# Performance work log

Hardware: AMD Instinct MI355X
Metric: run time of the kernel (lower is better)

## Reference

```python
import math
import jax, jax.numpy as jnp
import numpy as np

B, C, T = 4, 512, 1024
H = 8
KC = C // H
WIN = 4


def _get_relative_embeddings(emb, length):
    win = (emb.shape[1] - 1) // 2
    pad_length = max(length - (win + 1), 0)
    slice_start = max(win + 1 - length, 0)
    slice_end = slice_start + 2 * length - 1
    if pad_length > 0:
        emb = jnp.pad(emb, ((0, 0), (pad_length, pad_length), (0, 0)))
    return emb[:, slice_start:slice_end]


def _relative_to_absolute(x):
    # x: [b, h, L, 2L-1] -> [b, h, L, L] via skew trick
    b, h, L, _ = x.shape
    x = jnp.pad(x, ((0, 0), (0, 0), (0, 0), (0, 1)))          # [b,h,L,2L]
    x_flat = x.reshape(b, h, L * 2 * L)
    x_flat = jnp.pad(x_flat, ((0, 0), (0, 0), (0, L - 1)))    # [b,h,(L+1)(2L-1)]
    x_final = x_flat.reshape(b, h, L + 1, 2 * L - 1)
    return x_final[:, :, :L, L - 1:]


def _absolute_to_relative(x):
    # x: [b, h, L, L] -> [b, h, L, 2L-1]
    b, h, L, _ = x.shape
    x = jnp.pad(x, ((0, 0), (0, 0), (0, 0), (0, L - 1)))      # [b,h,L,2L-1]
    x_flat = x.reshape(b, h, L * (2 * L - 1))
    x_flat = jnp.pad(x_flat, ((0, 0), (0, 0), (L, 0)))        # [b,h,2L^2]
    x_final = x_flat.reshape(b, h, L, 2 * L)
    return x_final[:, :, :, 1:]


def setup_inputs() -> dict:
    key = jax.random.key(0)
    ks = jax.random.split(key, 12)
    xavier = math.sqrt(6.0 / (C + C))  # xavier_uniform for [C, C, 1] conv weight
    rel_std = KC ** (-0.5)
    return {
        "x": jax.random.normal(ks[0], (B, C, T), dtype=jnp.float32),
        "wq": jax.random.uniform(ks[1], (C, C), jnp.float32, -xavier, xavier),
        "bq": jnp.zeros((C,), jnp.float32),
        "wk": jax.random.uniform(ks[2], (C, C), jnp.float32, -xavier, xavier),
        "bk": jnp.zeros((C,), jnp.float32),
        "wv": jax.random.uniform(ks[3], (C, C), jnp.float32, -xavier, xavier),
        "bv": jnp.zeros((C,), jnp.float32),
        "wo": jax.random.normal(ks[4], (C, C), jnp.float32) * (1.0 / math.sqrt(C)),
        "bo": jnp.zeros((C,), jnp.float32),
        "emb_rel_k": jax.random.normal(ks[5], (1, 2 * WIN + 1, KC), jnp.float32) * rel_std,
        "emb_rel_v": jax.random.normal(ks[6], (1, 2 * WIN + 1, KC), jnp.float32) * rel_std,
    }


def reference(x, wq, bq, wk, bk, wv, bv, wo, bo, emb_rel_k, emb_rel_v):
    b, c, t = x.shape
    # 1x1 conv == channel matmul
    q = jnp.einsum("oi,bit->bot", wq, x) + bq[:, None]
    k = jnp.einsum("oi,bit->bot", wk, x) + bk[:, None]
    v = jnp.einsum("oi,bit->bot", wv, x) + bv[:, None]
    # [b, H, t, kc]
    q = q.reshape(b, H, KC, t).transpose(0, 1, 3, 2)
    k = k.reshape(b, H, KC, t).transpose(0, 1, 3, 2)
    v = v.reshape(b, H, KC, t).transpose(0, 1, 3, 2)
    inv_sqrt = 1.0 / math.sqrt(KC)
    scores = jnp.einsum("bhtc,bhsc->bhts", q, k) * inv_sqrt
    rel_k = _get_relative_embeddings(emb_rel_k, t)[0]            # [2t-1, kc]
    rel_logits = jnp.einsum("bhtc,rc->bhtr", q, rel_k)           # [b,h,t,2t-1]
    scores = scores + _relative_to_absolute(rel_logits) * inv_sqrt
    p_attn = jax.nn.softmax(scores, axis=-1)
    output = jnp.einsum("bhts,bhsc->bhtc", p_attn, v)
    rel_weights = _absolute_to_relative(p_attn)                  # [b,h,t,2t-1]
    rel_v = _get_relative_embeddings(emb_rel_v, t)[0]            # [2t-1, kc]
    output = output + jnp.einsum("bhtr,rc->bhtc", rel_weights, rel_v)
    output = output.transpose(0, 1, 3, 2).reshape(b, c, t)
    return jnp.einsum("oi,bit->bot", wo, output) + bo[:, None]
```

## Files before the change

kernel.cpp:

```cpp
#include <hip/hip_runtime.h>
#include <hip/hip_bf16.h>

#define Bdim 4
#define Cdim 512
#define Tdim 1024
#define Hn   8
#define KCd  64

typedef __attribute__((ext_vector_type(8))) short bf16x8;
typedef __attribute__((ext_vector_type(4))) float f32x4;

__device__ __forceinline__ unsigned short f32_bf16_rne(float f) {
    unsigned u = __float_as_uint(f);
    u += 0x7FFFu + ((u >> 16) & 1u);
    return (unsigned short)(u >> 16);
}
__device__ __forceinline__ float bf16_f32(unsigned short h) {
    return __uint_as_float(((unsigned)h) << 16);
}

__device__ __forceinline__ int off_row(int row, int c) {
    return (((row >> 4) * 2 + (c >> 5)) << 9)
         + (((((c >> 3) & 3) << 4) + (row & 15)) << 3) + (c & 7);
}
__device__ __forceinline__ int off_col(int c, int j) {
    return (((c >> 4) * 2 + (j >> 5)) << 9)
         + (((((j >> 3) & 3) << 4) + (c & 15)) << 3) + (j & 7);
}

__device__ __forceinline__ int sw(int row, int col) {
    return (row << 6) + ((((col >> 3) ^ (row & 7)) << 3) | (col & 7));
}
__device__ __forceinline__ bf16x8 fragld(const unsigned short* a, int row, int kstep, int quad) {
    return *(const bf16x8*)&a[(row << 6) + ((((kstep << 2) | quad) ^ (row & 7)) << 3)];
}

#define BM 128
#define BN 64
#define BK 32
#define LDK 40

__global__ __launch_bounds__(256) void gemm3_mfma(
    int mode,
    const float* __restrict__ w0, const float* __restrict__ w1, const float* __restrict__ w2,
    const float* __restrict__ b0, const float* __restrict__ b1, const float* __restrict__ b2,
    const float* __restrict__ x,
    unsigned short* __restrict__ qhi, unsigned short* __restrict__ qlo,
    unsigned short* __restrict__ khi, unsigned short* __restrict__ klo,
    unsigned short* __restrict__ vhi, unsigned short* __restrict__ vlo,
    float* __restrict__ ofp)
{
    __shared__ unsigned short Whi[BM][LDK], Wlo[BM][LDK];
    __shared__ unsigned short Xhi[BN][LDK], Xlo[BN][LDK];

    const int tid = threadIdx.x;

    int bx, by, b;
    {
        const int n = blockIdx.x;
        const int xcd = n & 7, slot = n >> 3;
        if (mode == 0) {
            const int stripe = (xcd << 3) | (slot / 12);
            by = slot % 12;
            bx = stripe & 15;
            b  = stripe >> 4;
        } else {
            const int stripe = (xcd << 3) | (slot >> 2);
            by = slot & 3;
            bx = stripe & 15;
            b  = stripe >> 4;
        }
    }

    const int m_tile = by * BM;
    const int sel = m_tile >> 9;
    const float* W  = sel == 0 ? w0 : (sel == 1 ? w1 : w2);
    const float* Bv = sel == 0 ? b0 : (sel == 1 ? b1 : b2);
    const int m0 = m_tile & 511;
    const int n0 = bx * BN;

    const float* Xb = x + (size_t)b * Cdim * Tdim;

    const int lane = tid & 63, wid = tid >> 6;
    const int wm = (wid & 1) * 64, wn = (wid >> 1) * 32;
    const int l15 = lane & 15, quad = lane >> 4;

    const int wk4 = (tid & 7) * 4;
    const int wmr = tid >> 3;
    const int xn  = tid & 63;
    const int xo  = tid >> 6;

    f32x4 acc[4][2];
    #pragma unroll
    for (int i = 0; i < 4; ++i)
        #pragma unroll
        for (int j = 0; j < 2; ++j) acc[i][j] = (f32x4){0.f, 0.f, 0.f, 0.f};

    for (int k0 = 0; k0 < Cdim; k0 += BK) {
        __syncthreads();

        #pragma unroll
        for (int p = 0; p < 4; ++p) {
            const int m = wmr + p * 32;
            float4 wv = *(const float4*)(W + (size_t)(m0 + m) * Cdim + k0 + wk4);
            ushort4 hi, lo;
            hi.x = f32_bf16_rne(wv.x); lo.x = f32_bf16_rne(wv.x - bf16_f32(hi.x));
            hi.y = f32_bf16_rne(wv.y); lo.y = f32_bf16_rne(wv.y - bf16_f32(hi.y));
            hi.z = f32_bf16_rne(wv.z); lo.z = f32_bf16_rne(wv.z - bf16_f32(hi.z));
            hi.w = f32_bf16_rne(wv.w); lo.w = f32_bf16_rne(wv.w - bf16_f32(hi.w));
            *(ushort4*)&Whi[m][wk4] = hi;
            *(ushort4*)&Wlo[m][wk4] = lo;
        }

        {
            float xv[8];
            #pragma unroll
            for (int kk = 0; kk < 8; ++kk)
                xv[kk] = Xb[(size_t)(k0 + xo * 8 + kk) * Tdim + n0 + xn];
            ushort4 hi0, hi1, lo0, lo1;
            unsigned short h;
            h = f32_bf16_rne(xv[0]); hi0.x = h; lo0.x = f32_bf16_rne(xv[0] - bf16_f32(h));
            h = f32_bf16_rne(xv[1]); hi0.y = h; lo0.y = f32_bf16_rne(xv[1] - bf16_f32(h));
            h = f32_bf16_rne(xv[2]); hi0.z = h; lo0.z = f32_bf16_rne(xv[2] - bf16_f32(h));
            h = f32_bf16_rne(xv[3]); hi0.w = h; lo0.w = f32_bf16_rne(xv[3] - bf16_f32(h));
            h = f32_bf16_rne(xv[4]); hi1.x = h; lo1.x = f32_bf16_rne(xv[4] - bf16_f32(h));
            h = f32_bf16_rne(xv[5]); hi1.y = h; lo1.y = f32_bf16_rne(xv[5] - bf16_f32(h));
            h = f32_bf16_rne(xv[6]); hi1.z = h; lo1.z = f32_bf16_rne(xv[6] - bf16_f32(h));
            h = f32_bf16_rne(xv[7]); hi1.w = h; lo1.w = f32_bf16_rne(xv[7] - bf16_f32(h));
            *(ushort4*)&Xhi[xn][xo * 8]     = hi0;
            *(ushort4*)&Xhi[xn][xo * 8 + 4] = hi1;
            *(ushort4*)&Xlo[xn][xo * 8]     = lo0;
            *(ushort4*)&Xlo[xn][xo * 8 + 4] = lo1;
        }
        __syncthreads();

        bf16x8 ahi[4], alo[4], bhi[2], blo[2];
        #pragma unroll
        for (int mt = 0; mt < 4; ++mt) {
            ahi[mt] = *(const bf16x8*)&Whi[wm + mt * 16 + l15][quad * 8];
            alo[mt] = *(const bf16x8*)&Wlo[wm + mt * 16 + l15][quad * 8];
        }
        #pragma unroll
        for (int nt = 0; nt < 2; ++nt) {
            bhi[nt] = *(const bf16x8*)&Xhi[wn + nt * 16 + l15][quad * 8];
            blo[nt] = *(const bf16x8*)&Xlo[wn + nt * 16 + l15][quad * 8];
        }
        #pragma unroll
        for (int mt = 0; mt < 4; ++mt)
            #pragma unroll
            for (int nt = 0; nt < 2; ++nt) {
                f32x4 c = acc[mt][nt];
                c = __builtin_amdgcn_mfma_f32_16x16x32_bf16(ahi[mt], bhi[nt], c, 0, 0, 0);
                c = __builtin_amdgcn_mfma_f32_16x16x32_bf16(ahi[mt], blo[nt], c, 0, 0, 0);
                c = __builtin_amdgcn_mfma_f32_16x16x32_bf16(alo[mt], bhi[nt], c, 0, 0, 0);
                acc[mt][nt] = c;
            }
    }

    if (mode == 1) {
        float* Ob = ofp + (size_t)b * Cdim * Tdim;
        #pragma unroll
        for (int mt = 0; mt < 4; ++mt) {
            const int mb = m0 + wm + mt * 16 + quad * 4;
            float bb[4];
            #pragma unroll
            for (int r = 0; r < 4; ++r) bb[r] = Bv[mb + r];
            #pragma unroll
            for (int nt = 0; nt < 2; ++nt) {
                const int t = n0 + wn + nt * 16 + l15;
                #pragma unroll
                for (int r = 0; r < 4; ++r)
                    Ob[(size_t)(mb + r) * Tdim + t] = acc[mt][nt][r] + bb[r];
            }
        }
    } else if (sel < 2) {
        unsigned short* phi = sel == 0 ? qhi : khi;
        unsigned short* plo = sel == 0 ? qlo : klo;
        #pragma unroll
        for (int mt = 0; mt < 4; ++mt) {
            const int mv = m0 + wm + mt * 16 + quad * 4;
            const int head = mv >> 6, c0 = mv & 63;
            float bb[4];
            #pragma unroll
            for (int r = 0; r < 4; ++r) bb[r] = Bv[mv + r];
            #pragma unroll
            for (int nt = 0; nt < 2; ++nt) {
                const int t = n0 + wn + nt * 16 + l15;
                const int tile = t >> 6, r_ = t & 63;
                const size_t off = (((size_t)(b * Hn + head) * 16 + tile) << 12)
                                 + (size_t)off_row(r_, c0);
                ushort4 h4, l4;
                float v0 = acc[mt][nt][0] + bb[0];
                float v1 = acc[mt][nt][1] + bb[1];
                float v2 = acc[mt][nt][2] + bb[2];
                float v3 = acc[mt][nt][3] + bb[3];
                h4.x = f32_bf16_rne(v0); l4.x = f32_bf16_rne(v0 - bf16_f32(h4.x));
                h4.y = f32_bf16_rne(v1); l4.y = f32_bf16_rne(v1 - bf16_f32(h4.y));
                h4.z = f32_bf16_rne(v2); l4.z = f32_bf16_rne(v2 - bf16_f32(h4.z));
                h4.w = f32_bf16_rne(v3); l4.w = f32_bf16_rne(v3 - bf16_f32(h4.w));
                *(ushort4*)(phi + off) = h4;
                *(ushort4*)(plo + off) = l4;
            }
        }
    } else {
        #pragma unroll
        for (int mt = 0; mt < 4; ++mt) {
            const int mv = m0 + wm + mt * 16 + quad * 4;
            const int head = mv >> 6;
            float bb[4];
            #pragma unroll
            for (int r = 0; r < 4; ++r) bb[r] = Bv[mv + r];
            #pragma unroll
            for (int nt = 0; nt < 2; ++nt) {
                const int t = n0 + wn + nt * 16 + l15;
                const int tile = t >> 6, jl = t & 63;
                const size_t tb = ((size_t)(b * Hn + head) * 16 + tile) << 12;
                #pragma unroll
                for (int r = 0; r < 4; ++r) {
                    const int cr = (mv & 63) + r;
                    const float v = acc[mt][nt][r] + bb[r];
                    const unsigned short h = f32_bf16_rne(v);
                    const size_t off = tb + off_col(cr, jl);
                    vhi[off] = h;
                    vlo[off] = f32_bf16_rne(v - bf16_f32(h));
                }
            }
        }
    }
}

__global__ __launch_bounds__(256) void attn_mfma(
    const unsigned short* __restrict__ qhi, const unsigned short* __restrict__ qlo,
    const unsigned short* __restrict__ khi, const unsigned short* __restrict__ klo,
    const unsigned short* __restrict__ vhi, const unsigned short* __restrict__ vlo,
    const float* __restrict__ ek,
    const float* __restrict__ ev,
    float* __restrict__ ctx)
{
    __shared__ alignas(16) unsigned short psh[4096], psl[4096];
    __shared__ float rk[576];
    __shared__ float evs[576];

    const int tid = threadIdx.x;

    int it, h, b;
    {
        const int n = blockIdx.x;
        const int xcd = n & 7, slot = n >> 3;
        const int pair = (xcd << 2) | (slot >> 4);
        it = slot & 15;
        b = pair >> 3;
        h = pair & 7;
    }
    const int i0 = it * 64;
    const int lane = tid & 63, w = tid >> 6;
    const int l15 = lane & 15, quad = lane >> 4;
    const int m_blk = w * 16 + l15;
    const int lo8 = lane << 3;

    const size_t bh16 = (size_t)(b * Hn + h) * 16;
    float* ctxb = ctx + ((size_t)b * Cdim + h * KCd) * Tdim;

    bf16x8 qfh[2], qfl[2];
    {
        const unsigned short* qth = qhi + ((bh16 + it) << 12);
        const unsigned short* qtl = qlo + ((bh16 + it) << 12);
        #pragma unroll
        for (int ks = 0; ks < 2; ++ks) {
            qfh[ks] = *(const bf16x8*)(qth + (((w << 1) | ks) << 9) + lo8);
            qfl[ks] = *(const bf16x8*)(qtl + (((w << 1) | ks) << 9) + lo8);
        }
    }

    bf16x8 ekh[2], ekl[2];
    #pragma unroll
    for (int ks = 0; ks < 2; ++ks) {
        #pragma unroll
        for (int j = 0; j < 8; ++j) { ekh[ks][j] = 0; ekl[ks][j] = 0; }
        if (l15 < 9) {
            #pragma unroll
            for (int j = 0; j < 8; ++j) {
                const float v = ek[l15 * 64 + ks * 32 + quad * 8 + j];
                const unsigned short hh = f32_bf16_rne(v);
                ekh[ks][j] = (short)hh;
                ekl[ks][j] = (short)f32_bf16_rne(v - bf16_f32(hh));
            }
        }
    }

    {
        f32x4 rkD = (f32x4){0.f, 0.f, 0.f, 0.f};
        #pragma unroll
        for (int ks = 0; ks < 2; ++ks) {
            rkD = __builtin_amdgcn_mfma_f32_16x16x32_bf16(qfh[ks], ekh[ks], rkD, 0, 0, 0);
            rkD = __builtin_amdgcn_mfma_f32_16x16x32_bf16(qfh[ks], ekl[ks], rkD, 0, 0, 0);
            rkD = __builtin_amdgcn_mfma_f32_16x16x32_bf16(qfl[ks], ekh[ks], rkD, 0, 0, 0);
        }
        if (l15 < 9) {
            #pragma unroll
            for (int r = 0; r < 4; ++r)
                rk[(w * 16 + quad * 4 + r) * 9 + l15] = rkD[r];
        }
    }
    for (int idx = tid; idx < 576; idx += 256) evs[idx] = ev[idx];
    __syncthreads();

    float m_run = -1e30f, l_run = 0.f;
    f32x4 Oc[4];
    #pragma unroll
    for (int ct = 0; ct < 4; ++ct) Oc[ct] = (f32x4){0.f, 0.f, 0.f, 0.f};

    const unsigned short* kh0 = khi + (bh16 << 12);
    const unsigned short* kl0 = klo + (bh16 << 12);
    const unsigned short* vh0 = vhi + (bh16 << 12);
    const unsigned short* vl0 = vlo + (bh16 << 12);

    for (int t = 0; t < 16; ++t) {
        const int j0 = t << 6;
        const size_t tb = (size_t)t << 12;
        const unsigned short* kht = kh0 + tb;
        const unsigned short* klt = kl0 + tb;
        const unsigned short* vht = vh0 + tb;
        const unsigned short* vlt = vl0 + tb;

        bf16x8 vbh[2][4], vbl[2][4];
        #pragma unroll
        for (int ks = 0; ks < 2; ++ks)
            #pragma unroll
            for (int ct = 0; ct < 4; ++ct) {
                vbh[ks][ct] = *(const bf16x8*)(vht + (((ct << 1) | ks) << 9) + lo8);
                vbl[ks][ct] = *(const bf16x8*)(vlt + (((ct << 1) | ks) << 9) + lo8);
            }

        f32x4 Sc[4];
        #pragma unroll
        for (int jt = 0; jt < 4; ++jt) Sc[jt] = (f32x4){0.f, 0.f, 0.f, 0.f};
        #pragma unroll
        for (int ks = 0; ks < 2; ++ks) {
            bf16x8 ah[4], al[4];
            #pragma unroll
            for (int jt = 0; jt < 4; ++jt) {
                ah[jt] = *(const bf16x8*)(kht + (((jt << 1) | ks) << 9) + lo8);
                al[jt] = *(const bf16x8*)(klt + (((jt << 1) | ks) << 9) + lo8);
            }
            #pragma unroll
            for (int jt = 0; jt < 4; ++jt) {
                Sc[jt] = __builtin_amdgcn_mfma_f32_16x16x32_bf16(ah[jt], qfh[ks], Sc[jt], 0, 0, 0);
                Sc[jt] = __builtin_amdgcn_mfma_f32_16x16x32_bf16(ah[jt], qfl[ks], Sc[jt], 0, 0, 0);
                Sc[jt] = __builtin_amdgcn_mfma_f32_16x16x32_bf16(al[jt], qfh[ks], Sc[jt], 0, 0, 0);
            }
        }

        const int dt = j0 - i0;
        const bool diag = (dt >= -67 && dt <= 67);
        if (diag) {
            #pragma unroll
            for (int jt = 0; jt < 4; ++jt) {
                const int db = dt + jt * 16 + quad * 4 - m_blk;
                #pragma unroll
                for (int r = 0; r < 4; ++r) {
                    const int d = db + r;
                    if ((unsigned)(d + 4) <= 8u) Sc[jt][r] += rk[m_blk * 9 + d + 4];
                }
            }
        }

        float mt = -1e30f;
        #pragma unroll
        for (int jt = 0; jt < 4; ++jt)
            #pragma unroll
            for (int r = 0; r < 4; ++r) {
                Sc[jt][r] *= 0.125f;
                mt = fmaxf(mt, Sc[jt][r]);
            }
        mt = fmaxf(mt, __shfl_xor(mt, 16));
        mt = fmaxf(mt, __shfl_xor(mt, 32));
        const float mn = fmaxf(m_run, mt);
        const float alpha = __expf(m_run - mn);
        float rs = 0.f;
        #pragma unroll
        for (int jt = 0; jt < 4; ++jt)
            #pragma unroll
            for (int r = 0; r < 4; ++r) {
                const float e = __expf(Sc[jt][r] - mn);
                Sc[jt][r] = e;
                rs += e;
            }
        rs += __shfl_xor(rs, 16);
        rs += __shfl_xor(rs, 32);
        l_run = l_run * alpha + rs;
        m_run = mn;

        #pragma unroll
        for (int jt = 0; jt < 4; ++jt) {
            ushort4 ph, pl;
            ph.x = f32_bf16_rne(Sc[jt][0]); pl.x = f32_bf16_rne(Sc[jt][0] - bf16_f32(ph.x));
            ph.y = f32_bf16_rne(Sc[jt][1]); pl.y = f32_bf16_rne(Sc[jt][1] - bf16_f32(ph.y));
            ph.z = f32_bf16_rne(Sc[jt][2]); pl.z = f32_bf16_rne(Sc[jt][2] - bf16_f32(ph.z));
            ph.w = f32_bf16_rne(Sc[jt][3]); pl.w = f32_bf16_rne(Sc[jt][3] - bf16_f32(ph.w));
            const int o = sw(m_blk, jt * 16 + quad * 4);
            *(ushort4*)&psh[o] = ph;
            *(ushort4*)&psl[o] = pl;
        }

        const float al0 = __shfl(alpha, quad * 4 + 0);
        const float al1 = __shfl(alpha, quad * 4 + 1);
        const float al2 = __shfl(alpha, quad * 4 + 2);
        const float al3 = __shfl(alpha, quad * 4 + 3);
        #pragma unroll
        for (int ct = 0; ct < 4; ++ct) {
            Oc[ct][0] *= al0; Oc[ct][1] *= al1; Oc[ct][2] *= al2; Oc[ct][3] *= al3;
        }
        #pragma unroll
        for (int ks = 0; ks < 2; ++ks) {
            bf16x8 pah = fragld(psh, m_blk, ks, quad);
            bf16x8 pal = fragld(psl, m_blk, ks, quad);
            #pragma unroll
            for (int ct = 0; ct < 4; ++ct) {
                Oc[ct] = __builtin_amdgcn_mfma_f32_16x16x32_bf16(pah, vbh[ks][ct], Oc[ct], 0, 0, 0);
                Oc[ct] = __builtin_amdgcn_mfma_f32_16x16x32_bf16(pah, vbl[ks][ct], Oc[ct], 0, 0, 0);
                Oc[ct] = __builtin_amdgcn_mfma_f32_16x16x32_bf16(pal, vbh[ks][ct], Oc[ct], 0, 0, 0);
            }
        }

        if (diag) {
            #pragma unroll
            for (int r = 0; r < 4; ++r) {
                const int mrow = w * 16 + quad * 4 + r;
                const int ig = i0 + mrow;
                #pragma unroll
                for (int e = 0; e < 9; ++e) {
                    const int jl = ig + e - 4 - j0;
                    if ((unsigned)jl < 64u) {
                        const int o = sw(mrow, jl);
                        const float p = bf16_f32(psh[o]) + bf16_f32(psl[o]);
                        #pragma unroll
                        for (int ct = 0; ct < 4; ++ct)
                            Oc[ct][r] += p * evs[e * 64 + ct * 16 + l15];
                    }
                }
            }
        }
    }

    const float rlv = 1.f / l_run;
    const float rl0 = __shfl(rlv, quad * 4 + 0);
    const float rl1 = __shfl(rlv, quad * 4 + 1);
    const float rl2 = __shfl(rlv, quad * 4 + 2);
    const float rl3 = __shfl(rlv, quad * 4 + 3);
    #pragma unroll
    for (int ct = 0; ct < 4; ++ct) {
        float4 o4;
        o4.x = Oc[ct][0] * rl0;
        o4.y = Oc[ct][1] * rl1;
        o4.z = Oc[ct][2] * rl2;
        o4.w = Oc[ct][3] * rl3;
        *(float4*)(ctxb + (size_t)(ct * 16 + l15) * Tdim + i0 + w * 16 + quad * 4) = o4;
    }
}

extern "C" void kernel_launch(void* const* d_in, const int* in_sizes, int n_in,
                              void* d_out, int out_size, void* d_ws, size_t ws_size,
                              hipStream_t stream) {
    const float* x  = (const float*)d_in[0];
    const float* wq = (const float*)d_in[1];
    const float* bq = (const float*)d_in[2];
    const float* wk = (const float*)d_in[3];
    const float* bk = (const float*)d_in[4];
    const float* wv = (const float*)d_in[5];
    const float* bv = (const float*)d_in[6];
    const float* wo = (const float*)d_in[7];
    const float* bo = (const float*)d_in[8];
    const float* ek = (const float*)d_in[9];
    const float* ev = (const float*)d_in[10];
    float* out = (float*)d_out;

    const size_t plane = (size_t)Bdim * Cdim * Tdim;
    unsigned short* qhi = (unsigned short*)d_ws;
    unsigned short* qlo = qhi + plane;
    unsigned short* khi = qlo + plane;
    unsigned short* klo = khi + plane;
    unsigned short* vhi = klo + plane;
    unsigned short* vlo = vhi + plane;
    float* cbuf = (float*)(vlo + plane);

    gemm3_mfma<<<dim3(768), 256, 0, stream>>>(
        0, wq, wk, wv, bq, bk, bv, x, qhi, qlo, khi, klo, vhi, vlo, nullptr);

    attn_mfma<<<dim3(512), 256, 0, stream>>>(
        qhi, qlo, khi, klo, vhi, vlo, ek, ev, cbuf);

    gemm3_mfma<<<dim3(256), 256, 0, stream>>>(
        1, wo, wo, wo, bo, bo, bo, cbuf,
        nullptr, nullptr, nullptr, nullptr, nullptr, nullptr, out);
}
```

Before: 182.8 us.

## Pre-split operands into MFMA fragment layout and drop LDS staging in GEMMs

Adds a prep kernel that converts all four weight matrices and x into hi/lo bf16 pairs, stored directly in MFMA fragment order. The projection GEMMs then load fragments straight from global memory with register double-buffering, and each wave computes a 64x64 tile with no shared memory or barriers. The attention kernel now writes its context as pre-split bf16 fragments, so the output projection also skips conversion. The cost is an extra launch plus more global traffic. Occupancy is lower (384 and 128 blocks), and the weights are re-split on every call.

```diff
diff --git a/kernel.cpp b/kernel.cpp
--- a/kernel.cpp
+++ b/kernel.cpp
@@ -18,14 +18,13 @@
 __device__ __forceinline__ float bf16_f32(unsigned short h) {
     return __uint_as_float(((unsigned)h) << 16);
 }
-
-__device__ __forceinline__ int off_row(int row, int c) {
-    return (((row >> 4) * 2 + (c >> 5)) << 9)
-         + (((((c >> 3) & 3) << 4) + (row & 15)) << 3) + (c & 7);
-}
-__device__ __forceinline__ int off_col(int c, int j) {
-    return (((c >> 4) * 2 + (j >> 5)) << 9)
-         + (((((j >> 3) & 3) << 4) + (c & 15)) << 3) + (j & 7);
+__device__ __forceinline__ void split8(const float* f, bf16x8& h8, bf16x8& l8) {
+    #pragma unroll
+    for (int e = 0; e < 8; ++e) {
+        const unsigned short hh = f32_bf16_rne(f[e]);
+        h8[e] = (short)hh;
+        l8[e] = (short)f32_bf16_rne(f[e] - bf16_f32(hh));
+    }
 }
 
 __device__ __forceinline__ int sw(int row, int col) {
@@ -35,124 +34,132 @@
     return *(const bf16x8*)&a[(row << 6) + ((((kstep << 2) | quad) ^ (row & 7)) << 3)];
 }
 
-#define BM 128
-#define BN 64
-#define BK 32
-#define LDK 40
-
-__global__ __launch_bounds__(256) void gemm3_mfma(
+
+__global__ __launch_bounds__(256) void prep_kernel(
+    const float* __restrict__ wq, const float* __restrict__ wk,
+    const float* __restrict__ wv, const float* __restrict__ wo,
+    const float* __restrict__ x,
+    unsigned short* __restrict__ WAhi, unsigned short* __restrict__ WAlo,
+    unsigned short* __restrict__ XBhi, unsigned short* __restrict__ XBlo)
+{
+    const int w = threadIdx.x >> 6, lane = threadIdx.x & 63;
+    const int l15 = lane & 15, quad = lane >> 4;
+    const int task = blockIdx.x * 4 + w;
+
+    if (task < 2048) {
+        const int mtile = task >> 4, kt = task & 15;
+        const int sel = mtile >> 5;
+        const float* W = sel == 0 ? wq : (sel == 1 ? wk : (sel == 2 ? wv : wo));
+        const int row = (mtile & 31) * 16 + l15;
+        const float* p = W + (size_t)row * Cdim + kt * 32 + quad * 8;
+        float f[8];
+        *(float4*)&f[0] = *(const float4*)p;
+        *(float4*)&f[4] = *(const float4*)(p + 4);
+        bf16x8 h8, l8;
+        split8(f, h8, l8);
+        const size_t base = (size_t)task * 512 + lane * 8;
+        *(bf16x8*)(WAhi + base) = h8;
+        *(bf16x8*)(WAlo + base) = l8;
+    } else {
+        const int t2 = task - 2048;
+        const int b = t2 >> 10, ntile = (t2 >> 4) & 63, kt = t2 & 15;
+        const float* Xb = x + (size_t)b * Cdim * Tdim;
+        const int n = ntile * 16 + l15;
+        const int k0 = kt * 32 + quad * 8;
+        float f[8];
+        #pragma unroll
+        for (int e = 0; e < 8; ++e) f[e] = Xb[(size_t)(k0 + e) * Tdim + n];
+        bf16x8 h8, l8;
+        split8(f, h8, l8);
+        const size_t base = (size_t)t2 * 512 + lane * 8;
+        *(bf16x8*)(XBhi + base) = h8;
+        *(bf16x8*)(XBlo + base) = l8;
+    }
+}
+
+__global__ __launch_bounds__(256) void gemm_mfma(
     int mode,
-    const float* __restrict__ w0, const float* __restrict__ w1, const float* __restrict__ w2,
+    const unsigned short* __restrict__ Ahi, const unsigned short* __restrict__ Alo,
+    const unsigned short* __restrict__ Bhi, const unsigned short* __restrict__ Blo,
     const float* __restrict__ b0, const float* __restrict__ b1, const float* __restrict__ b2,
-    const float* __restrict__ x,
     unsigned short* __restrict__ qhi, unsigned short* __restrict__ qlo,
     unsigned short* __restrict__ khi, unsigned short* __restrict__ klo,
     unsigned short* __restrict__ vhi, unsigned short* __restrict__ vlo,
     float* __restrict__ ofp)
 {
-    __shared__ unsigned short Whi[BM][LDK], Wlo[BM][LDK];
-    __shared__ unsigned short Xhi[BN][LDK], Xlo[BN][LDK];
-
     const int tid = threadIdx.x;
-
-    int bx, by, b;
+    const int w = tid >> 6, lane = tid & 63;
+    const int l15 = lane & 15, quad = lane >> 4;
+    const int lo8 = lane << 3;
+
+    int b, n64, m64, mtb, sel;
     {
-        const int n = blockIdx.x;
-        const int xcd = n & 7, slot = n >> 3;
+        const int id = blockIdx.x;
+        const int xcd = id & 7, slot = id >> 3;
         if (mode == 0) {
-            const int stripe = (xcd << 3) | (slot / 12);
-            by = slot % 12;
-            bx = stripe & 15;
-            b  = stripe >> 4;
+            const int col = xcd * 8 + slot / 6;
+            const int mg = slot % 6;
+            b = col >> 4; n64 = col & 15;
+            m64 = mg * 4 + w;
+            mtb = m64 * 4;
+            sel = m64 >> 3;
         } else {
-            const int stripe = (xcd << 3) | (slot >> 2);
-            by = slot & 3;
-            bx = stripe & 15;
-            b  = stripe >> 4;
-        }
-    }
-
-    const int m_tile = by * BM;
-    const int sel = m_tile >> 9;
-    const float* W  = sel == 0 ? w0 : (sel == 1 ? w1 : w2);
-    const float* Bv = sel == 0 ? b0 : (sel == 1 ? b1 : b2);
-    const int m0 = m_tile & 511;
-    const int n0 = bx * BN;
-
-    const float* Xb = x + (size_t)b * Cdim * Tdim;
-
-    const int lane = tid & 63, wid = tid >> 6;
-    const int wm = (wid & 1) * 64, wn = (wid >> 1) * 32;
-    const int l15 = lane & 15, quad = lane >> 4;
-
-    const int wk4 = (tid & 7) * 4;
-    const int wmr = tid >> 3;
-    const int xn  = tid & 63;
-    const int xo  = tid >> 6;
-
-    f32x4 acc[4][2];
+            const int col = xcd * 8 + (slot >> 1);
+            const int mg = slot & 1;
+            b = col >> 4; n64 = col & 15;
+            m64 = mg * 4 + w;
+            mtb = 96 + m64 * 4;
+            sel = 0;
+        }
+    }
+    const int ntb = b * 64 + n64 * 4;
+
+    f32x4 acc[4][4];
     #pragma unroll
     for (int i = 0; i < 4; ++i)
         #pragma unroll
-        for (int j = 0; j < 2; ++j) acc[i][j] = (f32x4){0.f, 0.f, 0.f, 0.f};
-
-    for (int k0 = 0; k0 < Cdim; k0 += BK) {
-        __syncthreads();
-
-        #pragma unroll
-        for (int p = 0; p < 4; ++p) {
-            const int m = wmr + p * 32;
-            float4 wv = *(const float4*)(W + (size_t)(m0 + m) * Cdim + k0 + wk4);
-            ushort4 hi, lo;
-            hi.x = f32_bf16_rne(wv.x); lo.x = f32_bf16_rne(wv.x - bf16_f32(hi.x));
-            hi.y = f32_bf16_rne(wv.y); lo.y = f32_bf16_rne(wv.y - bf16_f32(hi.y));
-            hi.z = f32_bf16_rne(wv.z); lo.z = f32_bf16_rne(wv.z - bf16_f32(hi.z));
-            hi.w = f32_bf16_rne(wv.w); lo.w = f32_bf16_rne(wv.w - bf16_f32(hi.w));
-            *(ushort4*)&Whi[m][wk4] = hi;
-            *(ushort4*)&Wlo[m][wk4] = lo;
-        }
-
-        {
-            float xv[8];
-            #pragma unroll
-            for (int kk = 0; kk < 8; ++kk)
-                xv[kk] = Xb[(size_t)(k0 + xo * 8 + kk) * Tdim + n0 + xn];
-            ushort4 hi0, hi1, lo0, lo1;
-            unsigned short h;
-            h = f32_bf16_rne(xv[0]); hi0.x = h; lo0.x = f32_bf16_rne(xv[0] - bf16_f32(h));
-            h = f32_bf16_rne(xv[1]); hi0.y = h; lo0.y = f32_bf16_rne(xv[1] - bf16_f32(h));
-            h = f32_bf16_rne(xv[2]); hi0.z = h; lo0.z = f32_bf16_rne(xv[2] - bf16_f32(h));
-            h = f32_bf16_rne(xv[3]); hi0.w = h; lo0.w = f32_bf16_rne(xv[3] - bf16_f32(h));
-            h = f32_bf16_rne(xv[4]); hi1.x = h; lo1.x = f32_bf16_rne(xv[4] - bf16_f32(h));
-            h = f32_bf16_rne(xv[5]); hi1.y = h; lo1.y = f32_bf16_rne(xv[5] - bf16_f32(h));
-            h = f32_bf16_rne(xv[6]); hi1.z = h; lo1.z = f32_bf16_rne(xv[6] - bf16_f32(h));
-            h = f32_bf16_rne(xv[7]); hi1.w = h; lo1.w = f32_bf16_rne(xv[7] - bf16_f32(h));
-            *(ushort4*)&Xhi[xn][xo * 8]     = hi0;
-            *(ushort4*)&Xhi[xn][xo * 8 + 4] = hi1;
-            *(ushort4*)&Xlo[xn][xo * 8]     = lo0;
-            *(ushort4*)&Xlo[xn][xo * 8 + 4] = lo1;
-        }
-        __syncthreads();
-
-        bf16x8 ahi[4], alo[4], bhi[2], blo[2];
-        #pragma unroll
-        for (int mt = 0; mt < 4; ++mt) {
-            ahi[mt] = *(const bf16x8*)&Whi[wm + mt * 16 + l15][quad * 8];
-            alo[mt] = *(const bf16x8*)&Wlo[wm + mt * 16 + l15][quad * 8];
-        }
-        #pragma unroll
-        for (int nt = 0; nt < 2; ++nt) {
-            bhi[nt] = *(const bf16x8*)&Xhi[wn + nt * 16 + l15][quad * 8];
-            blo[nt] = *(const bf16x8*)&Xlo[wn + nt * 16 + l15][quad * 8];
+        for (int j = 0; j < 4; ++j) acc[i][j] = (f32x4){0.f, 0.f, 0.f, 0.f};
+
+    bf16x8 Ah[2][4], Al[2][4], Bh[2][4], Bl[2][4];
+
+    #pragma unroll
+    for (int mt = 0; mt < 4; ++mt) {
+        const size_t o = (size_t)(mtb + mt) * 8192 + lo8;
+        Ah[0][mt] = *(const bf16x8*)(Ahi + o);
+        Al[0][mt] = *(const bf16x8*)(Alo + o);
+    }
+    #pragma unroll
+    for (int nt = 0; nt < 4; ++nt) {
+        const size_t o = (size_t)(ntb + nt) * 8192 + lo8;
+        Bh[0][nt] = *(const bf16x8*)(Bhi + o);
+        Bl[0][nt] = *(const bf16x8*)(Blo + o);
+    }
+
+    for (int kt = 0; kt < 16; ++kt) {
+        const int cur = kt & 1, nxt = cur ^ 1;
+        if (kt < 15) {
+            const int kn = (kt + 1) * 512;
+            #pragma unroll
+            for (int mt = 0; mt < 4; ++mt) {
+                const size_t o = (size_t)(mtb + mt) * 8192 + kn + lo8;
+                Ah[nxt][mt] = *(const bf16x8*)(Ahi + o);
+                Al[nxt][mt] = *(const bf16x8*)(Alo + o);
+            }
+            #pragma unroll
+            for (int nt = 0; nt < 4; ++nt) {
+                const size_t o = (size_t)(ntb + nt) * 8192 + kn + lo8;
+                Bh[nxt][nt] = *(const bf16x8*)(Bhi + o);
+                Bl[nxt][nt] = *(const bf16x8*)(Blo + o);
+            }
         }
         #pragma unroll
         for (int mt = 0; mt < 4; ++mt)
             #pragma unroll
-            for (int nt = 0; nt < 2; ++nt) {
+            for (int nt = 0; nt < 4; ++nt) {
                 f32x4 c = acc[mt][nt];
-                c = __builtin_amdgcn_mfma_f32_16x16x32_bf16(ahi[mt], bhi[nt], c, 0, 0, 0);
-                c = __builtin_amdgcn_mfma_f32_16x16x32_bf16(ahi[mt], blo[nt], c, 0, 0, 0);
-                c = __builtin_amdgcn_mfma_f32_16x16x32_bf16(alo[mt], bhi[nt], c, 0, 0, 0);
+                c = __builtin_amdgcn_mfma_f32_16x16x32_bf16(Ah[cur][mt], Bh[cur][nt], c, 0, 0, 0);
+                c = __builtin_amdgcn_mfma_f32_16x16x32_bf16(Ah[cur][mt], Bl[cur][nt], c, 0, 0, 0);
+                c = __builtin_amdgcn_mfma_f32_16x16x32_bf16(Al[cur][mt], Bh[cur][nt], c, 0, 0, 0);
                 acc[mt][nt] = c;
             }
     }
@@ -161,68 +168,71 @@
         float* Ob = ofp + (size_t)b * Cdim * Tdim;
         #pragma unroll
         for (int mt = 0; mt < 4; ++mt) {
-            const int mb = m0 + wm + mt * 16 + quad * 4;
+            const int m = m64 * 64 + mt * 16 + quad * 4;
             float bb[4];
             #pragma unroll
-            for (int r = 0; r < 4; ++r) bb[r] = Bv[mb + r];
-            #pragma unroll
-            for (int nt = 0; nt < 2; ++nt) {
-                const int t = n0 + wn + nt * 16 + l15;
+            for (int r = 0; r < 4; ++r) bb[r] = b0[m + r];
+            #pragma unroll
+            for (int nt = 0; nt < 4; ++nt) {
+                const int t = n64 * 64 + nt * 16 + l15;
                 #pragma unroll
                 for (int r = 0; r < 4; ++r)
-                    Ob[(size_t)(mb + r) * Tdim + t] = acc[mt][nt][r] + bb[r];
+                    Ob[(size_t)(m + r) * Tdim + t] = acc[mt][nt][r] + bb[r];
             }
         }
     } else if (sel < 2) {
-        unsigned short* phi = sel == 0 ? qhi : khi;
-        unsigned short* plo = sel == 0 ? qlo : klo;
+        const float* Bv = sel == 0 ? b0 : b1;
+        unsigned short* ph = sel == 0 ? qhi : khi;
+        unsigned short* pl = sel == 0 ? qlo : klo;
         #pragma unroll
         for (int mt = 0; mt < 4; ++mt) {
-            const int mv = m0 + wm + mt * 16 + quad * 4;
-            const int head = mv >> 6, c0 = mv & 63;
+            const int mv = m64 * 64 + mt * 16 + quad * 4;
+            const int head = (mv >> 6) & 7;
+            const int c0 = mt * 16 + quad * 4;
             float bb[4];
             #pragma unroll
-            for (int r = 0; r < 4; ++r) bb[r] = Bv[mv + r];
-            #pragma unroll
-            for (int nt = 0; nt < 2; ++nt) {
-                const int t = n0 + wn + nt * 16 + l15;
-                const int tile = t >> 6, r_ = t & 63;
-                const size_t off = (((size_t)(b * Hn + head) * 16 + tile) << 12)
-                                 + (size_t)off_row(r_, c0);
+            for (int r = 0; r < 4; ++r) bb[r] = Bv[(mv & 511) + r];
+            const int lane_out = (((c0 >> 3) & 3) << 4) + l15;
+            const int e0 = c0 & 7;
+            const size_t tbase = (((size_t)(b * Hn + head) * 16 + n64) << 12);
+            #pragma unroll
+            for (int nt = 0; nt < 4; ++nt) {
+                const int g = nt * 2 + (mt >> 1);
+                const size_t off = tbase + g * 512 + lane_out * 8 + e0;
                 ushort4 h4, l4;
-                float v0 = acc[mt][nt][0] + bb[0];
-                float v1 = acc[mt][nt][1] + bb[1];
-                float v2 = acc[mt][nt][2] + bb[2];
-                float v3 = acc[mt][nt][3] + bb[3];
-                h4.x = f32_bf16_rne(v0); l4.x = f32_bf16_rne(v0 - bf16_f32(h4.x));
-                h4.y = f32_bf16_rne(v1); l4.y = f32_bf16_rne(v1 - bf16_f32(h4.y));
-                h4.z = f32_bf16_rne(v2); l4.z = f32_bf16_rne(v2 - bf16_f32(h4.z));
-                h4.w = f32_bf16_rne(v3); l4.w = f32_bf16_rne(v3 - bf16_f32(h4.w));
-                *(ushort4*)(phi + off) = h4;
-                *(ushort4*)(plo + off) = l4;
-            }
-        }
-    } else {
-        #pragma unroll
-        for (int mt = 0; mt < 4; ++mt) {
-            const int mv = m0 + wm + mt * 16 + quad * 4;
-            const int head = mv >> 6;
-            float bb[4];
-            #pragma unroll
-            for (int r = 0; r < 4; ++r) bb[r] = Bv[mv + r];
-            #pragma unroll
-            for (int nt = 0; nt < 2; ++nt) {
-                const int t = n0 + wn + nt * 16 + l15;
-                const int tile = t >> 6, jl = t & 63;
-                const size_t tb = ((size_t)(b * Hn + head) * 16 + tile) << 12;
                 #pragma unroll
                 for (int r = 0; r < 4; ++r) {
-                    const int cr = (mv & 63) + r;
                     const float v = acc[mt][nt][r] + bb[r];
-                    const unsigned short h = f32_bf16_rne(v);
-                    const size_t off = tb + off_col(cr, jl);
-                    vhi[off] = h;
-                    vlo[off] = f32_bf16_rne(v - bf16_f32(h));
+                    const unsigned short hh = f32_bf16_rne(v);
+                    ((unsigned short*)&h4)[r] = hh;
+                    ((unsigned short*)&l4)[r] = f32_bf16_rne(v - bf16_f32(hh));
+                }
+                *(ushort4*)(ph + off) = h4;
+                *(ushort4*)(pl + off) = l4;
+            }
+        }
+    } else {
+        #pragma unroll
+        for (int mt = 0; mt < 4; ++mt) {
+            const int mv = m64 * 64 + mt * 16 + quad * 4;
+            const int head = (mv >> 6) & 7;
+            float bb[4];
+            #pragma unroll
+            for (int r = 0; r < 4; ++r) bb[r] = b2[(mv & 511) + r];
+            const size_t tbase = (((size_t)(b * Hn + head) * 16 + n64) << 12);
+            #pragma unroll
+            for (int nt = 0; nt < 4; ++nt) {
+                const int tl = nt * 16 + l15;
+                const int g = mt * 2 + (tl >> 5);
+                const int lv0 = (((tl >> 3) & 3) << 4) + quad * 4;
+                const int e = tl & 7;
+                #pragma unroll
+                for (int r = 0; r < 4; ++r) {
+                    const float v = acc[mt][nt][r] + bb[r];
+                    const unsigned short hh = f32_bf16_rne(v);
+                    const size_t off = tbase + g * 512 + (size_t)(lv0 + r) * 8 + e;
+                    vhi[off] = hh;
+                    vlo[off] = f32_bf16_rne(v - bf16_f32(hh));
                 }
             }
         }
@@ -235,14 +245,13 @@
     const unsigned short* __restrict__ vhi, const unsigned short* __restrict__ vlo,
     const float* __restrict__ ek,
     const float* __restrict__ ev,
-    float* __restrict__ ctx)
+    unsigned short* __restrict__ cxhi, unsigned short* __restrict__ cxlo)
 {
     __shared__ alignas(16) unsigned short psh[4096], psl[4096];
     __shared__ float rk[576];
     __shared__ float evs[576];
 
     const int tid = threadIdx.x;
-
     int it, h, b;
     {
         const int n = blockIdx.x;
@@ -259,7 +268,6 @@
     const int lo8 = lane << 3;
 
     const size_t bh16 = (size_t)(b * Hn + h) * 16;
-    float* ctxb = ctx + ((size_t)b * Cdim + h * KCd) * Tdim;
 
     bf16x8 qfh[2], qfl[2];
     {
@@ -444,18 +452,27 @@
     }
 
     const float rlv = 1.f / l_run;
-    const float rl0 = __shfl(rlv, quad * 4 + 0);
-    const float rl1 = __shfl(rlv, quad * 4 + 1);
-    const float rl2 = __shfl(rlv, quad * 4 + 2);
-    const float rl3 = __shfl(rlv, quad * 4 + 3);
+    float rl[4];
+    rl[0] = __shfl(rlv, quad * 4 + 0);
+    rl[1] = __shfl(rlv, quad * 4 + 1);
+    rl[2] = __shfl(rlv, quad * 4 + 2);
+    rl[3] = __shfl(rlv, quad * 4 + 3);
+    const int ntile16 = it * 4 + w;
+    const int e = l15 & 7;
     #pragma unroll
     for (int ct = 0; ct < 4; ++ct) {
-        float4 o4;
-        o4.x = Oc[ct][0] * rl0;
-        o4.y = Oc[ct][1] * rl1;
-        o4.z = Oc[ct][2] * rl2;
-        o4.w = Oc[ct][3] * rl3;
-        *(float4*)(ctxb + (size_t)(ct * 16 + l15) * Tdim + i0 + w * 16 + quad * 4) = o4;
+        const int cl = ct * 16 + l15;
+        const int ktc = h * 2 + (cl >> 5);
+        const int lane_c = (((ct * 2 + (l15 >> 3)) & 3) << 4) + quad * 4;
+        const size_t base = (((size_t)(b * 64 + ntile16)) * 16 + ktc) * 512;
+        #pragma unroll
+        for (int r = 0; r < 4; ++r) {
+            const float v = Oc[ct][r] * rl[r];
+            const unsigned short hh = f32_bf16_rne(v);
+            const size_t off = base + (size_t)(lane_c + r) * 8 + e;
+            cxhi[off] = hh;
+            cxlo[off] = f32_bf16_rne(v - bf16_f32(hh));
+        }
     }
 }
 
@@ -475,22 +492,32 @@
     const float* ev = (const float*)d_in[10];
     float* out = (float*)d_out;
 
-    const size_t plane = (size_t)Bdim * Cdim * Tdim;
-    unsigned short* qhi = (unsigned short*)d_ws;
-    unsigned short* qlo = qhi + plane;
-    unsigned short* khi = qlo + plane;
-    unsigned short* klo = khi + plane;
-    unsigned short* vhi = klo + plane;
-    unsigned short* vlo = vhi + plane;
-    float* cbuf = (float*)(vlo + plane);
-
-    gemm3_mfma<<<dim3(768), 256, 0, stream>>>(
-        0, wq, wk, wv, bq, bk, bv, x, qhi, qlo, khi, klo, vhi, vlo, nullptr);
+    const size_t PW = 2048u * 512u;
+    const size_t PX = 4u * 1024u * 512u;
+    unsigned short* WAhi = (unsigned short*)d_ws;
+    unsigned short* WAlo = WAhi + PW;
+    unsigned short* XBhi = WAlo + PW;
+    unsigned short* XBlo = XBhi + PX;
+    unsigned short* qhi  = XBlo + PX;
+    unsigned short* qlo  = qhi + PX;
+    unsigned short* khi  = qlo + PX;
+    unsigned short* klo  = khi + PX;
+    unsigned short* vhi  = klo + PX;
+    unsigned short* vlo  = vhi + PX;
+    unsigned short* cxhi = vlo + PX;
+    unsigned short* cxlo = cxhi + PX;
+
+    prep_kernel<<<dim3(1536), 256, 0, stream>>>(
+        wq, wk, wv, wo, x, WAhi, WAlo, XBhi, XBlo);
+
+    gemm_mfma<<<dim3(384), 256, 0, stream>>>(
+        0, WAhi, WAlo, XBhi, XBlo, bq, bk, bv,
+        qhi, qlo, khi, klo, vhi, vlo, nullptr);
 
     attn_mfma<<<dim3(512), 256, 0, stream>>>(
-        qhi, qlo, khi, klo, vhi, vlo, ek, ev, cbuf);
-
-    gemm3_mfma<<<dim3(256), 256, 0, stream>>>(
-        1, wo, wo, wo, bo, bo, bo, cbuf,
+        qhi, qlo, khi, klo, vhi, vlo, ek, ev, cxhi, cxlo);
+
+    gemm_mfma<<<dim3(128), 256, 0, stream>>>(
+        1, WAhi, WAlo, cxhi, cxlo, bo, bo, bo,
         nullptr, nullptr, nullptr, nullptr, nullptr, nullptr, out);
 }
```

After: 199.9 us. 9.4% more time.
